# Performance work log

Measured on AMD Instinct MI355X. Metric: run time of the kernel, lower is better.

The kernel has to match this reference:

```python
import jax, jax.numpy as jnp
import numpy as np

N = 100000
E = 3200000
G = 64  # number of graphs in the batch


def gat_layer(x, edge_index, edge_attr, W, a_src, a_dst, We, a_e, b, n):
    """Single-head PyG GATConv with edge features.
    add_self_loops=True, fill_value='mean', negative_slope=0.2.
    Returns (out [n,C], new_edge_index [2,E+n], alpha [E+n,1])."""
    src, dst = edge_index[0], edge_index[1]
    # self-loop edge_attr = mean of incoming edge attrs (fill_value='mean')
    deg = jax.ops.segment_sum(jnp.ones_like(dst, dtype=edge_attr.dtype), dst, n)
    loop_attr = jax.ops.segment_sum(edge_attr, dst, n) / jnp.maximum(deg, 1.0)[:, None]
    loop = jnp.arange(n, dtype=src.dtype)
    src = jnp.concatenate([src, loop])
    dst = jnp.concatenate([dst, loop])
    ea = jnp.concatenate([edge_attr, loop_attr], axis=0)  # [E+n, edge_dim]
    h = x @ W                                             # [n, C]
    asrc = h @ a_src                                      # [n]
    adst = h @ a_dst                                      # [n]
    ae = (ea @ We) @ a_e                                  # [E+n]
    alpha = jax.nn.leaky_relu(asrc[src] + adst[dst] + ae, negative_slope=0.2)
    # segment softmax over destination nodes (every node has a self-loop)
    amax = jax.ops.segment_max(alpha, dst, n)
    ex = jnp.exp(alpha - amax[dst])
    denom = jax.ops.segment_sum(ex, dst, n)
    alpha = ex / (denom[dst] + 1e-16)
    out = jax.ops.segment_sum(alpha[:, None] * h[src], dst, n) + b
    return out, jnp.stack([src, dst]), alpha[:, None]


def setup_inputs() -> dict:
    key = jax.random.key(0)
    ks = jax.random.split(key, 24)
    s = 0.1
    inp = {
        "x": jax.random.normal(ks[0], (N, 5), jnp.float32),
        "edge_index": jax.random.randint(ks[1], (2, E), 0, N, jnp.int32),
        "edge_attr": jax.random.normal(ks[2], (E, 3), jnp.float32),
        "batch": jnp.sort(jax.random.randint(ks[3], (N,), 0, G, jnp.int32)),
        # conv1: in=5 -> 64, edge_dim=3
        "W1": jax.random.normal(ks[4], (5, 64), jnp.float32) * s,
        "as1": jax.random.normal(ks[5], (64,), jnp.float32) * s,
        "ad1": jax.random.normal(ks[6], (64,), jnp.float32) * s,
        "We1": jax.random.normal(ks[7], (3, 64), jnp.float32) * s,
        "ae1": jax.random.normal(ks[8], (64,), jnp.float32) * s,
        "b1": jnp.zeros((64,), jnp.float32),
        # conv2: 64 -> 64, edge_dim=1
        "W2": jax.random.normal(ks[9], (64, 64), jnp.float32) * s,
        "as2": jax.random.normal(ks[10], (64,), jnp.float32) * s,
        "ad2": jax.random.normal(ks[11], (64,), jnp.float32) * s,
        "We2": jax.random.normal(ks[12], (1, 64), jnp.float32) * s,
        "ae2": jax.random.normal(ks[13], (64,), jnp.float32) * s,
        "b2": jnp.zeros((64,), jnp.float32),
        # conv3: 64 -> 32, edge_dim=1
        "W3": jax.random.normal(ks[14], (64, 32), jnp.float32) * s,
        "as3": jax.random.normal(ks[15], (32,), jnp.float32) * s,
        "ad3": jax.random.normal(ks[16], (32,), jnp.float32) * s,
        "We3": jax.random.normal(ks[17], (1, 32), jnp.float32) * s,
        "ae3": jax.random.normal(ks[18], (32,), jnp.float32) * s,
        "b3": jnp.zeros((32,), jnp.float32),
    }
    return inp


def reference(x, edge_index, edge_attr, batch,
              W1, as1, ad1, We1, ae1, b1,
              W2, as2, ad2, We2, ae2, b2,
              W3, as3, ad3, We3, ae3, b3):
    h, ei, alpha = gat_layer(x, edge_index, edge_attr, W1, as1, ad1, We1, ae1, b1, N)
    h = jax.nn.relu(h)
    h, ei, alpha = gat_layer(h, ei, alpha, W2, as2, ad2, We2, ae2, b2, N)
    h = jax.nn.relu(h)
    h, _, _ = gat_layer(h, ei, alpha, W3, as3, ad3, We3, ae3, b3, N)
    # global mean pool over graphs
    cnt = jax.ops.segment_sum(jnp.ones((N,), h.dtype), batch, G)
    out = jax.ops.segment_sum(h, batch, G) / jnp.maximum(cnt, 1.0)[:, None]
    return out  # [G, 32]
```

## Files before the change

### kernel.cpp

```cpp
#include <hip/hip_runtime.h>
#include <hip/hip_fp16.h>

#define LRELU(x) ((x) > 0.f ? (x) : 0.2f * (x))
#define SBSH 9
#define SBN 512
#define NB1 256
#define MAXSB 1024
#define PC 16

__global__ void small_weights_k(const float* __restrict__ We1, const float* __restrict__ ae1,
                                const float* __restrict__ We2, const float* __restrict__ ae2,
                                const float* __restrict__ We3, const float* __restrict__ ae3,
                                float* __restrict__ sw) {
  int t = threadIdx.x;
  float v0 = We1[t] * ae1[t];
  float v1 = We1[64 + t] * ae1[t];
  float v2 = We1[128 + t] * ae1[t];
  float v3 = We2[t] * ae2[t];
  float v4 = (t < 32) ? We3[t] * ae3[t] : 0.f;
#pragma unroll
  for (int off = 32; off > 0; off >>= 1) {
    v0 += __shfl_down(v0, off);
    v1 += __shfl_down(v1, off);
    v2 += __shfl_down(v2, off);
    v3 += __shfl_down(v3, off);
    v4 += __shfl_down(v4, off);
  }
  if (t == 0) { sw[0] = v0; sw[1] = v1; sw[2] = v2; sw[3] = v3; sw[4] = v4; }
}

__global__ __launch_bounds__(256) void count1_k(const int* __restrict__ dst,
                                                int* __restrict__ gcnt, int E, int NSB) {
  __shared__ int cnt[MAXSB];
  const int t = threadIdx.x, blk = blockIdx.x;
  for (int i = t; i < NSB; i += 256) cnt[i] = 0;
  __syncthreads();
  const int CE = (E + NB1 - 1) / NB1;
  const int e0 = blk * CE, e1 = min(E, e0 + CE);
  for (int e = e0 + t; e < e1; e += 256) {
    int d = __builtin_nontemporal_load(&dst[e]);
    atomicAdd(&cnt[d >> SBSH], 1);
  }
  __syncthreads();
  for (int i = t; i < NSB; i += 256) gcnt[i * NB1 + blk] = cnt[i];
}

__global__ __launch_bounds__(1024) void scanA_k(const int* __restrict__ gcnt,
                                                int* __restrict__ gbase,
                                                int* __restrict__ bsum, int M) {
  __shared__ int s[1024];
  const int t = threadIdx.x;
  const int i = blockIdx.x * 1024 + t;
  int v = (i < M) ? gcnt[i] : 0;
  s[t] = v;
  __syncthreads();
  for (int off = 1; off < 1024; off <<= 1) {
    int add = (t >= off) ? s[t - off] : 0;
    __syncthreads();
    s[t] += add;
    __syncthreads();
  }
  if (i < M) gbase[i] = s[t] - v;
  if (t == 1023) bsum[blockIdx.x] = s[t];
}

__global__ void scanB_k(const int* __restrict__ bsum, int* __restrict__ boff, int nb) {
  if (threadIdx.x == 0) {
    int acc = 0;
    for (int b = 0; b < nb; b++) { boff[b] = acc; acc += bsum[b]; }
  }
}

__global__ void scanC_k(int* __restrict__ gbase, const int* __restrict__ boff,
                        int* __restrict__ rowptr, int M, int E) {
  int i = blockIdx.x * 256 + threadIdx.x;
  if (i < M) gbase[i] += boff[i >> 10];
  if (i == 0) { gbase[M] = E; rowptr[0] = 0; }
}

__global__ __launch_bounds__(256) void append2_k(
    const int* __restrict__ src, const int* __restrict__ dst,
    const float* __restrict__ eattr, const int* __restrict__ gbase,
    int2* __restrict__ recDS, const float* __restrict__ sw, int E, int NSB) {
  __shared__ int base[MAXSB];
  __shared__ int off[MAXSB];
  const int t = threadIdx.x, blk = blockIdx.x;
  for (int i = t; i < NSB; i += 256) { base[i] = gbase[i * NB1 + blk]; off[i] = 0; }
  __syncthreads();
  const float w0 = sw[0], w1 = sw[1], w2 = sw[2];
  const int CE = (E + NB1 - 1) / NB1;
  const int e0 = blk * CE, e1 = min(E, e0 + CE);
  for (int e = e0 + t; e < e1; e += 256) {
    int d = __builtin_nontemporal_load(&dst[e]);
    int sv = __builtin_nontemporal_load(&src[e]);
    float a0 = __builtin_nontemporal_load(&eattr[e * 3]);
    float a1 = __builtin_nontemporal_load(&eattr[e * 3 + 1]);
    float a2 = __builtin_nontemporal_load(&eattr[e * 3 + 2]);
    float ae = a0 * w0 + a1 * w1 + a2 * w2;
    int sb = d >> SBSH;
    int pos = base[sb] + atomicAdd(&off[sb], 1);
    recDS[pos] = make_int2((int)(((unsigned)(d & (SBN - 1)) << 23) | (unsigned)sv),
                           __float_as_int(ae));
  }
}

__global__ __launch_bounds__(1024) void sb_build_k(
    const int2* __restrict__ recDS, const int* __restrict__ gbase,
    const float* __restrict__ asrc, const float* __restrict__ adst,
    int* __restrict__ rowptr, float* __restrict__ asum, float* __restrict__ esum,
    int2* __restrict__ edge, int n, int NSB) {
  __shared__ int cnt[SBN];
  __shared__ int sc[SBN];
  __shared__ int fill[SBN];
  __shared__ float adl[SBN];
  __shared__ float rs[SBN];
  __shared__ float es[SBN];
  const int t = threadIdx.x, sb = blockIdx.x;
  const int v0 = sb << SBSH;
  const int nloc = min(SBN, n - v0);
  if (t < SBN) {
    cnt[t] = 0; fill[t] = 0; rs[t] = 0.f; es[t] = 0.f;
    adl[t] = (t < nloc) ? adst[v0 + t] : 0.f;
  }
  __syncthreads();
  const int seg0 = gbase[sb * NB1], seg1 = gbase[(sb + 1) * NB1];
  for (int i = seg0 + t; i < seg1; i += 1024)
    atomicAdd(&cnt[(unsigned)recDS[i].x >> 23], 1);
  __syncthreads();
  if (t < SBN) sc[t] = cnt[t];
  __syncthreads();
  for (int off = 1; off < SBN; off <<= 1) {
    int add = (t < SBN && t >= off) ? sc[t - off] : 0;
    __syncthreads();
    if (t < SBN) sc[t] += add;
    __syncthreads();
  }
  if (t < nloc) rowptr[v0 + t + 1] = seg0 + sc[t];
  for (int i = seg0 + t; i < seg1; i += 1024) {
    int2 rec = recDS[i];
    unsigned q = (unsigned)rec.x;
    float ae = __int_as_float(rec.y);
    int loc = q >> 23;
    int sv = (int)(q & 0x7FFFFFu);
    int pos = seg0 + (sc[loc] - cnt[loc]) + atomicAdd(&fill[loc], 1);
    float ex = __expf(LRELU(asrc[sv] + adl[loc] + ae));
    edge[pos] = make_int2(sv, __float_as_int(ex));
    atomicAdd(&rs[loc], ae);
    atomicAdd(&es[loc], ex);
  }
  __syncthreads();
  if (t < nloc) { asum[v0 + t] = rs[t]; esum[v0 + t] = es[t]; }
}


__global__ void gemm1_k(const float* __restrict__ x, const float* __restrict__ W,
                        const float* __restrict__ as, const float* __restrict__ ad,
                        __half* __restrict__ h, float* __restrict__ asrc,
                        float* __restrict__ adst, int n) {
  int lane = threadIdx.x & 63;
  int v = (blockIdx.x * blockDim.x + threadIdx.x) >> 6;
  if (v >= n) return;
  float acc = 0.f;
#pragma unroll
  for (int k = 0; k < 5; k++) acc += x[v * 5 + k] * W[k * 64 + lane];
  h[(size_t)v * 64 + lane] = __float2half(acc);
  float ps = acc * as[lane], pd = acc * ad[lane];
#pragma unroll
  for (int off = 32; off > 0; off >>= 1) {
    ps += __shfl_down(ps, off);
    pd += __shfl_down(pd, off);
  }
  if (lane == 0) { asrc[v] = ps; adst[v] = pd; }
}


template <int C>
__global__ __launch_bounds__(256) void gemm_tile_k(
    const float* __restrict__ x, const float* __restrict__ W,
    const float* __restrict__ as, const float* __restrict__ ad,
    __half* __restrict__ h, float* __restrict__ asrc, float* __restrict__ adst, int n) {
  constexpr int NT = 4096 / C;
  constexpr int CG = C / 4;
  constexpr int XTP = NT + 4;
  __shared__ float XT[64][XTP];
  __shared__ float Wl[64 * C];
  const int t = threadIdx.x;
  const int v0 = blockIdx.x * NT;
  for (int i = t; i < 64 * C; i += 256) Wl[i] = W[i];
  for (int i = t; i < NT * 64; i += 256) {
    int node = i >> 6, k = i & 63;
    int v = v0 + node;
    XT[k][node] = (v < n) ? x[(size_t)v * 64 + k] : 0.f;
  }
  __syncthreads();
  const int cg = t % CG, ng = t / CG;
  const int c0 = cg * 4, n0 = ng * 4;
  float acc[4][4] = {};
#pragma unroll 4
  for (int k = 0; k < 64; ++k) {
    const float4 xv = *(const float4*)&XT[k][n0];
    const float4 wv = *(const float4*)&Wl[k * C + c0];
    acc[0][0] += xv.x * wv.x; acc[0][1] += xv.x * wv.y; acc[0][2] += xv.x * wv.z; acc[0][3] += xv.x * wv.w;
    acc[1][0] += xv.y * wv.x; acc[1][1] += xv.y * wv.y; acc[1][2] += xv.y * wv.z; acc[1][3] += xv.y * wv.w;
    acc[2][0] += xv.z * wv.x; acc[2][1] += xv.z * wv.y; acc[2][2] += xv.z * wv.z; acc[2][3] += xv.z * wv.w;
    acc[3][0] += xv.w * wv.x; acc[3][1] += xv.w * wv.y; acc[3][2] += xv.w * wv.z; acc[3][3] += xv.w * wv.w;
  }
  float asv[4] = {as[c0], as[c0 + 1], as[c0 + 2], as[c0 + 3]};
  float adv[4] = {ad[c0], ad[c0 + 1], ad[c0 + 2], ad[c0 + 3]};
  float ps[4], pd[4];
#pragma unroll
  for (int ni = 0; ni < 4; ++ni) {
    ps[ni] = acc[ni][0] * asv[0] + acc[ni][1] * asv[1] + acc[ni][2] * asv[2] + acc[ni][3] * asv[3];
    pd[ni] = acc[ni][0] * adv[0] + acc[ni][1] * adv[1] + acc[ni][2] * adv[2] + acc[ni][3] * adv[3];
  }
#pragma unroll
  for (int off = CG / 2; off > 0; off >>= 1) {
#pragma unroll
    for (int ni = 0; ni < 4; ++ni) {
      ps[ni] += __shfl_xor(ps[ni], off);
      pd[ni] += __shfl_xor(pd[ni], off);
    }
  }
#pragma unroll
  for (int ni = 0; ni < 4; ++ni) {
    int v = v0 + n0 + ni;
    if (v < n) {
      union { __half hh[4]; uint2 u; } pk;
      pk.hh[0] = __float2half(acc[ni][0]);
      pk.hh[1] = __float2half(acc[ni][1]);
      pk.hh[2] = __float2half(acc[ni][2]);
      pk.hh[3] = __float2half(acc[ni][3]);
      *(uint2*)&h[(size_t)v * C + c0] = pk.u;
      if (cg == 0) { asrc[v] = ps[ni]; adst[v] = pd[ni]; }
    }
  }
}

__device__ __forceinline__ void fma8(float2* acc, float e, const uint4& u) {
  float2 f0 = __half22float2(*(const __half2*)&u.x);
  float2 f1 = __half22float2(*(const __half2*)&u.y);
  float2 f2 = __half22float2(*(const __half2*)&u.z);
  float2 f3 = __half22float2(*(const __half2*)&u.w);
  acc[0].x += e * f0.x; acc[0].y += e * f0.y;
  acc[1].x += e * f1.x; acc[1].y += e * f1.y;
  acc[2].x += e * f2.x; acc[2].y += e * f2.y;
  acc[3].x += e * f3.x; acc[3].y += e * f3.y;
}

template <int LAYER, int C>
__global__ __launch_bounds__(256) void agg_k(
    const int* __restrict__ rowptr, int2* __restrict__ edge,
    const __half* __restrict__ h, const float* __restrict__ asrc,
    const float* __restrict__ adst, const float* __restrict__ asum,
    const float* __restrict__ esum, const float* __restrict__ pinv,
    const float* __restrict__ lp1, const float* __restrict__ lp2,
    float* __restrict__ oinv, float* __restrict__ ol1, float* __restrict__ ol2,
    const float* __restrict__ sw, const float* __restrict__ bias,
    float* __restrict__ out, int n) {
  constexpr int L = (C == 64) ? 64 : 32;
  constexpr int LPE = C / 8;
  constexpr int EPI = L / LPE;
  const int lane = threadIdx.x & 63;
  const int ln = lane & (L - 1);
  const int wid = (blockIdx.x * blockDim.x + threadIdx.x) >> 6;
  const int v = (C == 64) ? wid : wid * 2 + (lane >> 5);
  if (v >= n) return;
  const float s = (LAYER == 1) ? 1.f : (LAYER == 2 ? sw[3] : sw[4]);
  const float fac = (LAYER == 1) ? 1.f : pinv[v];
  const float sf = s * fac;
  const int r0 = rowptr[v], r1 = rowptr[v + 1];
  const float av_d = adst[v], av_s = asrc[v];

  float rawsum = 0.f, den = 0.f;
  if (LAYER >= 2) {
    for (int p = r0 + ln; p < r1; p += L) {
      int2 pk = edge[p];
      float a = __int_as_float(pk.y);
      rawsum += a;
      float lg = asrc[pk.x] + av_d + sf * a;
      float ex = __expf(LRELU(lg));
      edge[p].y = __float_as_int(ex);
      den += ex;
    }
    __threadfence_block();
#pragma unroll
    for (int off = L / 2; off > 0; off >>= 1) {
      den += __shfl_xor(den, off);
      rawsum += __shfl_xor(rawsum, off);
    }
  } else {
    den = esum[v];
  }
  const float base = av_s + av_d;
  float la1 = 0.f, la2 = 0.f, e1 = 0.f, e2 = 0.f;
  if (LAYER >= 2) { la1 = fac * lp1[v]; e1 = __expf(LRELU(base + s * la1)); den += e1; }
  if (LAYER >= 3) { la2 = fac * lp2[v]; e2 = __expf(LRELU(base + s * la2)); den += e2; }
  int dd = (r1 - r0) + (LAYER - 1);
  if (dd < 1) dd = 1;
  float sum_a = (LAYER == 1) ? asum[v] : fac * rawsum + la1 + la2;
  float lmean = sum_a / (float)dd;
  float exm = __expf(LRELU(base + s * lmean));
  den += exm;
  float inv = 1.f / (den + 1e-16f);
  if (ln == 0) {
    if (LAYER < 3) oinv[v] = inv;
    if (LAYER == 1) ol1[v] = exm;
    if (LAYER == 2) { ol1[v] = e1; ol2[v] = exm; }
  }

  const int g = ln / LPE;
  const int q = ln % LPE;
  const uint4* __restrict__ h4 = (const uint4*)h;
  float2 accA[4] = {{0.f,0.f},{0.f,0.f},{0.f,0.f},{0.f,0.f}};
  float2 accB[4] = {{0.f,0.f},{0.f,0.f},{0.f,0.f},{0.f,0.f}};
  int p = r0;
  for (; p + 2 * EPI <= r1; p += 2 * EPI) {
    int2 rA = edge[p + g];
    int2 rB = edge[p + EPI + g];
    uint4 uA = h4[rA.x * LPE + q];
    uint4 uB = h4[rB.x * LPE + q];
    fma8(accA, __int_as_float(rA.y), uA);
    fma8(accB, __int_as_float(rB.y), uB);
  }
  for (; p < r1; p += EPI) {
    int idx = p + g;
    float e_;
    int2 rr;
    if (idx < r1) { rr = edge[idx]; e_ = __int_as_float(rr.y); }
    else { rr = edge[r1 - 1]; e_ = 0.f; }
    uint4 u = h4[rr.x * LPE + q];
    fma8(accA, e_, u);
  }
#pragma unroll
  for (int j = 0; j < 4; ++j) {
    accA[j].x += accB[j].x;
    accA[j].y += accB[j].y;
  }
#pragma unroll
  for (int off = LPE; off < L; off <<= 1) {
#pragma unroll
    for (int j = 0; j < 4; ++j) {
      accA[j].x += __shfl_xor(accA[j].x, off);
      accA[j].y += __shfl_xor(accA[j].y, off);
    }
  }
  if (g == 0) {
    uint4 uh = h4[v * LPE + q];
    float2 f0 = __half22float2(*(const __half2*)&uh.x);
    float2 f1 = __half22float2(*(const __half2*)&uh.y);
    float2 f2 = __half22float2(*(const __half2*)&uh.z);
    float2 f3 = __half22float2(*(const __half2*)&uh.w);
    float sl = e1 + e2 + exm;
    float4 b0 = *(const float4*)&bias[q * 8];
    float4 b1 = *(const float4*)&bias[q * 8 + 4];
    float4 o0, o1;
    o0.x = (accA[0].x + sl * f0.x) * inv + b0.x;
    o0.y = (accA[0].y + sl * f0.y) * inv + b0.y;
    o0.z = (accA[1].x + sl * f1.x) * inv + b0.z;
    o0.w = (accA[1].y + sl * f1.y) * inv + b0.w;
    o1.x = (accA[2].x + sl * f2.x) * inv + b1.x;
    o1.y = (accA[2].y + sl * f2.y) * inv + b1.y;
    o1.z = (accA[3].x + sl * f3.x) * inv + b1.z;
    o1.w = (accA[3].y + sl * f3.y) * inv + b1.w;
    if (LAYER < 3) {
      o0.x = fmaxf(o0.x, 0.f); o0.y = fmaxf(o0.y, 0.f);
      o0.z = fmaxf(o0.z, 0.f); o0.w = fmaxf(o0.w, 0.f);
      o1.x = fmaxf(o1.x, 0.f); o1.y = fmaxf(o1.y, 0.f);
      o1.z = fmaxf(o1.z, 0.f); o1.w = fmaxf(o1.w, 0.f);
    }
    *(float4*)&out[(size_t)v * C + q * 8] = o0;
    *(float4*)&out[(size_t)v * C + q * 8 + 4] = o1;
  }
}


__global__ __launch_bounds__(256) void poolA_k(const float* __restrict__ h,
                                               const int* __restrict__ batch,
                                               float* __restrict__ partial, int n) {
  const int b = blockIdx.x;
  const int g = b / PC, ch = b % PC;
  int lo = 0, hi = n;
  while (lo < hi) { int m = (lo + hi) >> 1; if (batch[m] < g) lo = m + 1; else hi = m; }
  const int start = lo;
  hi = n;
  while (lo < hi) { int m = (lo + hi) >> 1; if (batch[m] < g + 1) lo = m + 1; else hi = m; }
  const int end = lo;
  const int len = end - start;
  const int c0 = start + (int)((long long)len * ch / PC);
  const int c1 = start + (int)((long long)len * (ch + 1) / PC);
  const int t = threadIdx.x;
  const int c = t & 31, r = t >> 5;
  float acc = 0.f;
  for (int v = c0 + r; v < c1; v += 8) acc += h[(size_t)v * 32 + c];
  __shared__ float sm[256];
  sm[t] = acc;
  __syncthreads();
  if (t < 128) sm[t] += sm[t + 128];
  __syncthreads();
  if (t < 64) sm[t] += sm[t + 64];
  __syncthreads();
  if (t < 32) partial[(b << 5) + t] = sm[t] + sm[t + 32];
}

__global__ void poolB_k(const float* __restrict__ partial, const int* __restrict__ batch,
                        float* __restrict__ out, int n) {
  const int g = blockIdx.x;
  const int t = threadIdx.x;
  if (t >= 32) return;
  int lo = 0, hi = n;
  while (lo < hi) { int m = (lo + hi) >> 1; if (batch[m] < g) lo = m + 1; else hi = m; }
  const int start = lo;
  hi = n;
  while (lo < hi) { int m = (lo + hi) >> 1; if (batch[m] < g + 1) lo = m + 1; else hi = m; }
  const int cnt = lo - start;
  float acc = 0.f;
#pragma unroll
  for (int ch = 0; ch < PC; ++ch) acc += partial[((g * PC + ch) << 5) + t];
  out[g * 32 + t] = acc / (float)(cnt > 0 ? cnt : 1);
}


extern "C" void kernel_launch(void* const* d_in, const int* in_sizes, int n_in,
                              void* d_out, int out_size, void* d_ws, size_t ws_size,
                              hipStream_t stream) {
  const float* x     = (const float*)d_in[0];
  const int*   ei    = (const int*)d_in[1];
  const float* eattr = (const float*)d_in[2];
  const int*   batch = (const int*)d_in[3];
  const float *W1 = (const float*)d_in[4],  *as1 = (const float*)d_in[5],
              *ad1 = (const float*)d_in[6], *We1 = (const float*)d_in[7],
              *ae1 = (const float*)d_in[8], *b1  = (const float*)d_in[9];
  const float *W2 = (const float*)d_in[10], *as2 = (const float*)d_in[11],
              *ad2 = (const float*)d_in[12], *We2 = (const float*)d_in[13],
              *ae2 = (const float*)d_in[14], *b2  = (const float*)d_in[15];
  const float *W3 = (const float*)d_in[16], *as3 = (const float*)d_in[17],
              *ad3 = (const float*)d_in[18], *We3 = (const float*)d_in[19],
              *ae3 = (const float*)d_in[20], *b3  = (const float*)d_in[21];

  const int n = in_sizes[3];
  const int E = in_sizes[1] / 2;
  const int G = out_size / 32;
  const int* srcp = ei;
  const int* dstp = ei + E;
  const int NSB = (n + SBN - 1) >> SBSH;
  const int M = NSB * NB1;
  const int NBL = (M + 1023) / 1024;

  char* w = (char*)d_ws;
  auto alloc = [&](size_t bytes) -> void* {
    void* p = (void*)w;
    w += (bytes + 255) & ~(size_t)255;
    return p;
  };
  size_t blob_sz = (size_t)E * 8 > (size_t)n * 256 ? (size_t)E * 8 : (size_t)n * 256;
  char* blob = (char*)alloc(blob_sz);
  int2*  recDS = (int2*)blob;
  float* O     = (float*)blob;
  int2*  edge  = (int2*)alloc((size_t)E * 8);
  __half* H    = (__half*)alloc((size_t)n * 64 * 2);
  int*   gcnt  = (int*)alloc((size_t)M * 4);
  int*   gbase = (int*)alloc((size_t)(M + 1) * 4);
  int*   bsum  = (int*)alloc((size_t)NBL * 4 + 256);
  int*   boff  = (int*)alloc((size_t)NBL * 4 + 256);
  int*   rowptr= (int*)alloc((size_t)(n + 1) * 4);
  float* asum  = (float*)alloc((size_t)n * 4);
  float* esum  = (float*)alloc((size_t)n * 4);
  float* asrcB = (float*)alloc((size_t)n * 4);
  float* adstB = (float*)alloc((size_t)n * 4);
  float* loopA = (float*)alloc((size_t)n * 4);
  float* loopB1= (float*)alloc((size_t)n * 4);
  float* loopB2= (float*)alloc((size_t)n * 4);
  float* invA  = (float*)alloc((size_t)n * 4);
  float* invB  = (float*)alloc((size_t)n * 4);
  float* sw    = (float*)alloc(256);
  float* part  = (float*)alloc((size_t)G * PC * 32 * 4);

  dim3 blk256(256);
  dim3 gWave((n + 3) / 4);
  const int nw3 = (n + 1) / 2;
  dim3 gWave3((nw3 + 3) / 4);

  small_weights_k<<<1, 64, 0, stream>>>(We1, ae1, We2, ae2, We3, ae3, sw);
  count1_k<<<NB1, blk256, 0, stream>>>(dstp, gcnt, E, NSB);
  scanA_k<<<NBL, 1024, 0, stream>>>(gcnt, gbase, bsum, M);
  scanB_k<<<1, 64, 0, stream>>>(bsum, boff, NBL);
  scanC_k<<<dim3((M + 256) / 256), blk256, 0, stream>>>(gbase, boff, rowptr, M, E);
  append2_k<<<NB1, blk256, 0, stream>>>(srcp, dstp, eattr, gbase, recDS, sw, E, NSB);
  gemm1_k<<<gWave, blk256, 0, stream>>>(x, W1, as1, ad1, H, asrcB, adstB, n);
  sb_build_k<<<NSB, 1024, 0, stream>>>(recDS, gbase, asrcB, adstB,
                                       rowptr, asum, esum, edge, n, NSB);
  agg_k<1, 64><<<gWave, blk256, 0, stream>>>(rowptr, edge, H, asrcB, adstB, asum, esum,
                                             nullptr, nullptr, nullptr,
                                             invA, loopA, nullptr, sw, b1, O, n);
  gemm_tile_k<64><<<dim3((n + 63) / 64), blk256, 0, stream>>>(O, W2, as2, ad2, H, asrcB, adstB, n);
  agg_k<2, 64><<<gWave, blk256, 0, stream>>>(rowptr, edge, H, asrcB, adstB, nullptr, nullptr,
                                             invA, loopA, nullptr,
                                             invB, loopB1, loopB2, sw, b2, O, n);
  gemm_tile_k<32><<<dim3((n + 127) / 128), blk256, 0, stream>>>(O, W3, as3, ad3, H, asrcB, adstB, n);
  agg_k<3, 32><<<gWave3, blk256, 0, stream>>>(rowptr, edge, H, asrcB, adstB, nullptr, nullptr,
                                              invB, loopB1, loopB2,
                                              nullptr, nullptr, nullptr, sw, b3, O, n);
  poolA_k<<<dim3(G * PC), blk256, 0, stream>>>(O, batch, part, n);
  poolB_k<<<G, 64, 0, stream>>>(part, batch, (float*)d_out, n);
}
```

Before: 424.2 us.

## Store intermediate layer outputs in fp16 and vectorize edge passes

Layer 1 and 2 aggregation outputs (post-ReLU) are now written as fp16, and the following tile GEMM reads them as half2 and converts to float, halving that intermediate traffic. The layer 2/3 logit pass handles two packed edges per lane with int4 loads and stores. The gather loop is unrolled to four edges per iteration and uses nontemporal loads for edge records. The cost is fp16 rounding of hidden activations, plus extra register pressure from the deeper unroll.

Result: slower. 486.5 us (+14.7%).

```diff
diff --git a/kernel.cpp b/kernel.cpp
--- a/kernel.cpp
+++ b/kernel.cpp
@@ -7,6 +7,8 @@
 #define NB1 256
 #define MAXSB 1024
 #define PC 16
+
+typedef unsigned long long ull;
 
 __global__ void small_weights_k(const float* __restrict__ We1, const float* __restrict__ ae1,
                                 const float* __restrict__ We2, const float* __restrict__ ae2,
@@ -176,7 +178,7 @@
 
 template <int C>
 __global__ __launch_bounds__(256) void gemm_tile_k(
-    const float* __restrict__ x, const float* __restrict__ W,
+    const __half* __restrict__ x, const float* __restrict__ W,
     const float* __restrict__ as, const float* __restrict__ ad,
     __half* __restrict__ h, float* __restrict__ asrc, float* __restrict__ adst, int n) {
   constexpr int NT = 4096 / C;
@@ -187,10 +189,13 @@
   const int t = threadIdx.x;
   const int v0 = blockIdx.x * NT;
   for (int i = t; i < 64 * C; i += 256) Wl[i] = W[i];
-  for (int i = t; i < NT * 64; i += 256) {
-    int node = i >> 6, k = i & 63;
+  for (int i = t; i < NT * 32; i += 256) {
+    int node = i >> 5, kk = (i & 31) << 1;
     int v = v0 + node;
-    XT[k][node] = (v < n) ? x[(size_t)v * 64 + k] : 0.f;
+    unsigned u = (v < n) ? *(const unsigned*)&x[(size_t)v * 64 + kk] : 0u;
+    float2 f = __half22float2(*(const __half2*)&u);
+    XT[kk][node] = f.x;
+    XT[kk + 1][node] = f.y;
   }
   __syncthreads();
   const int cg = t % CG, ng = t / CG;
@@ -256,7 +261,7 @@
     const float* __restrict__ lp1, const float* __restrict__ lp2,
     float* __restrict__ oinv, float* __restrict__ ol1, float* __restrict__ ol2,
     const float* __restrict__ sw, const float* __restrict__ bias,
-    float* __restrict__ out, int n) {
+    void* __restrict__ outv, int n) {
   constexpr int L = (C == 64) ? 64 : 32;
   constexpr int LPE = C / 8;
   constexpr int EPI = L / LPE;
@@ -273,14 +278,37 @@
 
   float rawsum = 0.f, den = 0.f;
   if (LAYER >= 2) {
-    for (int p = r0 + ln; p < r1; p += L) {
-      int2 pk = edge[p];
-      float a = __int_as_float(pk.y);
-      rawsum += a;
-      float lg = asrc[pk.x] + av_d + sf * a;
-      float ex = __expf(LRELU(lg));
-      edge[p].y = __float_as_int(ex);
-      den += ex;
+    int pa = r0;
+    if (pa & 1) {
+      if (ln == 0) {
+        int2 pk = edge[pa];
+        float a = __int_as_float(pk.y);
+        rawsum += a;
+        float ex = __expf(LRELU(asrc[pk.x] + av_d + sf * a));
+        edge[pa].y = __float_as_int(ex);
+        den += ex;
+      }
+      pa++;
+    }
+    for (int p = pa + 2 * ln; p < r1; p += 2 * L) {
+      if (p + 1 < r1) {
+        int4 q = *(const int4*)&edge[p];
+        float a0 = __int_as_float(q.y), a1 = __int_as_float(q.w);
+        rawsum += a0 + a1;
+        float ex0 = __expf(LRELU(asrc[q.x] + av_d + sf * a0));
+        float ex1 = __expf(LRELU(asrc[q.z] + av_d + sf * a1));
+        q.y = __float_as_int(ex0);
+        q.w = __float_as_int(ex1);
+        *(int4*)&edge[p] = q;
+        den += ex0 + ex1;
+      } else {
+        int2 pk = edge[p];
+        float a = __int_as_float(pk.y);
+        rawsum += a;
+        float ex = __expf(LRELU(asrc[pk.x] + av_d + sf * a));
+        edge[p].y = __float_as_int(ex);
+        den += ex;
+      }
     }
     __threadfence_block();
 #pragma unroll
@@ -311,37 +339,43 @@
   const int g = ln / LPE;
   const int q = ln % LPE;
   const uint4* __restrict__ h4 = (const uint4*)h;
-  float2 accA[4] = {{0.f,0.f},{0.f,0.f},{0.f,0.f},{0.f,0.f}};
-  float2 accB[4] = {{0.f,0.f},{0.f,0.f},{0.f,0.f},{0.f,0.f}};
+  float2 A0[4] = {{0.f,0.f},{0.f,0.f},{0.f,0.f},{0.f,0.f}};
+  float2 A1[4] = {{0.f,0.f},{0.f,0.f},{0.f,0.f},{0.f,0.f}};
   int p = r0;
-  for (; p + 2 * EPI <= r1; p += 2 * EPI) {
-    int2 rA = edge[p + g];
-    int2 rB = edge[p + EPI + g];
-    uint4 uA = h4[rA.x * LPE + q];
-    uint4 uB = h4[rB.x * LPE + q];
-    fma8(accA, __int_as_float(rA.y), uA);
-    fma8(accB, __int_as_float(rB.y), uB);
-  }
-  for (; p < r1; p += EPI) {
+  for (; p + 4 * EPI <= r1; p += 4 * EPI) {
+    ull q0 = __builtin_nontemporal_load((const ull*)&edge[p + g]);
+    ull q1 = __builtin_nontemporal_load((const ull*)&edge[p + EPI + g]);
+    ull q2 = __builtin_nontemporal_load((const ull*)&edge[p + 2 * EPI + g]);
+    ull q3 = __builtin_nontemporal_load((const ull*)&edge[p + 3 * EPI + g]);
+    uint4 u0 = h4[(int)(unsigned)q0 * LPE + q];
+    uint4 u1 = h4[(int)(unsigned)q1 * LPE + q];
+    uint4 u2 = h4[(int)(unsigned)q2 * LPE + q];
+    uint4 u3 = h4[(int)(unsigned)q3 * LPE + q];
+    fma8(A0, __uint_as_float((unsigned)(q0 >> 32)), u0);
+    fma8(A1, __uint_as_float((unsigned)(q1 >> 32)), u1);
+    fma8(A0, __uint_as_float((unsigned)(q2 >> 32)), u2);
+    fma8(A1, __uint_as_float((unsigned)(q3 >> 32)), u3);
+  }
+  for (; p + EPI <= r1; p += EPI) {
+    ull qq = __builtin_nontemporal_load((const ull*)&edge[p + g]);
+    uint4 u = h4[(int)(unsigned)qq * LPE + q];
+    fma8(A0, __uint_as_float((unsigned)(qq >> 32)), u);
+  }
+  if (p < r1) {
     int idx = p + g;
-    float e_;
-    int2 rr;
-    if (idx < r1) { rr = edge[idx]; e_ = __int_as_float(rr.y); }
-    else { rr = edge[r1 - 1]; e_ = 0.f; }
+    int2 rr = (idx < r1) ? edge[idx] : edge[r1 - 1];
+    float e_ = (idx < r1) ? __int_as_float(rr.y) : 0.f;
     uint4 u = h4[rr.x * LPE + q];
-    fma8(accA, e_, u);
-  }
-#pragma unroll
-  for (int j = 0; j < 4; ++j) {
-    accA[j].x += accB[j].x;
-    accA[j].y += accB[j].y;
-  }
+    fma8(A0, e_, u);
+  }
+#pragma unroll
+  for (int j = 0; j < 4; ++j) { A0[j].x += A1[j].x; A0[j].y += A1[j].y; }
 #pragma unroll
   for (int off = LPE; off < L; off <<= 1) {
 #pragma unroll
     for (int j = 0; j < 4; ++j) {
-      accA[j].x += __shfl_xor(accA[j].x, off);
-      accA[j].y += __shfl_xor(accA[j].y, off);
+      A0[j].x += __shfl_xor(A0[j].x, off);
+      A0[j].y += __shfl_xor(A0[j].y, off);
     }
   }
   if (g == 0) {
@@ -351,25 +385,26 @@
     float2 f2 = __half22float2(*(const __half2*)&uh.z);
     float2 f3 = __half22float2(*(const __half2*)&uh.w);
     float sl = e1 + e2 + exm;
-    float4 b0 = *(const float4*)&bias[q * 8];
-    float4 b1 = *(const float4*)&bias[q * 8 + 4];
-    float4 o0, o1;
-    o0.x = (accA[0].x + sl * f0.x) * inv + b0.x;
-    o0.y = (accA[0].y + sl * f0.y) * inv + b0.y;
-    o0.z = (accA[1].x + sl * f1.x) * inv + b0.z;
-    o0.w = (accA[1].y + sl * f1.y) * inv + b0.w;
-    o1.x = (accA[2].x + sl * f2.x) * inv + b1.x;
-    o1.y = (accA[2].y + sl * f2.y) * inv + b1.y;
-    o1.z = (accA[3].x + sl * f3.x) * inv + b1.z;
-    o1.w = (accA[3].y + sl * f3.y) * inv + b1.w;
+    float o[8];
+    o[0] = (A0[0].x + sl * f0.x) * inv + bias[q * 8 + 0];
+    o[1] = (A0[0].y + sl * f0.y) * inv + bias[q * 8 + 1];
+    o[2] = (A0[1].x + sl * f1.x) * inv + bias[q * 8 + 2];
+    o[3] = (A0[1].y + sl * f1.y) * inv + bias[q * 8 + 3];
+    o[4] = (A0[2].x + sl * f2.x) * inv + bias[q * 8 + 4];
+    o[5] = (A0[2].y + sl * f2.y) * inv + bias[q * 8 + 5];
+    o[6] = (A0[3].x + sl * f3.x) * inv + bias[q * 8 + 6];
+    o[7] = (A0[3].y + sl * f3.y) * inv + bias[q * 8 + 7];
     if (LAYER < 3) {
-      o0.x = fmaxf(o0.x, 0.f); o0.y = fmaxf(o0.y, 0.f);
-      o0.z = fmaxf(o0.z, 0.f); o0.w = fmaxf(o0.w, 0.f);
-      o1.x = fmaxf(o1.x, 0.f); o1.y = fmaxf(o1.y, 0.f);
-      o1.z = fmaxf(o1.z, 0.f); o1.w = fmaxf(o1.w, 0.f);
-    }
-    *(float4*)&out[(size_t)v * C + q * 8] = o0;
-    *(float4*)&out[(size_t)v * C + q * 8 + 4] = o1;
+      union { __half hh[8]; uint4 u; } pk;
+#pragma unroll
+      for (int j = 0; j < 8; ++j) pk.hh[j] = __float2half(fmaxf(o[j], 0.f));
+      *(uint4*)&((__half*)outv)[(size_t)v * C + q * 8] = pk.u;
+    } else {
+      float4 o0 = make_float4(o[0], o[1], o[2], o[3]);
+      float4 o1 = make_float4(o[4], o[5], o[6], o[7]);
+      *(float4*)&((float*)outv)[(size_t)v * C + q * 8] = o0;
+      *(float4*)&((float*)outv)[(size_t)v * C + q * 8 + 4] = o1;
+    }
   }
 }
 
@@ -452,10 +487,13 @@
     w += (bytes + 255) & ~(size_t)255;
     return p;
   };
-  size_t blob_sz = (size_t)E * 8 > (size_t)n * 256 ? (size_t)E * 8 : (size_t)n * 256;
+  size_t oh_bytes = ((size_t)n * 128 + 255) & ~(size_t)255;
+  size_t blob_sz = (size_t)E * 8;
+  if (blob_sz < oh_bytes + (size_t)n * 128) blob_sz = oh_bytes + (size_t)n * 128;
   char* blob = (char*)alloc(blob_sz);
-  int2*  recDS = (int2*)blob;
-  float* O     = (float*)blob;
+  int2*   recDS = (int2*)blob;
+  __half* Oh    = (__half*)blob;
+  float*  O32   = (float*)(blob + oh_bytes);
   int2*  edge  = (int2*)alloc((size_t)E * 8);
   __half* H    = (__half*)alloc((size_t)n * 64 * 2);
   int*   gcnt  = (int*)alloc((size_t)M * 4);
@@ -491,15 +529,15 @@
                                        rowptr, asum, esum, edge, n, NSB);
   agg_k<1, 64><<<gWave, blk256, 0, stream>>>(rowptr, edge, H, asrcB, adstB, asum, esum,
                                              nullptr, nullptr, nullptr,
-                                             invA, loopA, nullptr, sw, b1, O, n);
-  gemm_tile_k<64><<<dim3((n + 63) / 64), blk256, 0, stream>>>(O, W2, as2, ad2, H, asrcB, adstB, n);
+                                             invA, loopA, nullptr, sw, b1, (void*)Oh, n);
+  gemm_tile_k<64><<<dim3((n + 63) / 64), blk256, 0, stream>>>(Oh, W2, as2, ad2, H, asrcB, adstB, n);
   agg_k<2, 64><<<gWave, blk256, 0, stream>>>(rowptr, edge, H, asrcB, adstB, nullptr, nullptr,
                                              invA, loopA, nullptr,
-                                             invB, loopB1, loopB2, sw, b2, O, n);
-  gemm_tile_k<32><<<dim3((n + 127) / 128), blk256, 0, stream>>>(O, W3, as3, ad3, H, asrcB, adstB, n);
+                                             invB, loopB1, loopB2, sw, b2, (void*)Oh, n);
+  gemm_tile_k<32><<<dim3((n + 127) / 128), blk256, 0, stream>>>(Oh, W3, as3, ad3, H, asrcB, adstB, n);
   agg_k<3, 32><<<gWave3, blk256, 0, stream>>>(rowptr, edge, H, asrcB, adstB, nullptr, nullptr,
                                               invB, loopB1, loopB2,
-                                              nullptr, nullptr, nullptr, sw, b3, O, n);
-  poolA_k<<<dim3(G * PC), blk256, 0, stream>>>(O, batch, part, n);
+                                              nullptr, nullptr, nullptr, sw, b3, (void*)O32, n);
+  poolA_k<<<dim3(G * PC), blk256, 0, stream>>>(O32, batch, part, n);
   poolB_k<<<G, 64, 0, stream>>>(part, batch, (float*)d_out, n);
 }
```
